# Performance work log

Hardware: AMD Instinct MI355X
Metric: run time of the kernel (lower is better)

The kernel has to match this reference:

```python
import jax, jax.numpy as jnp
import numpy as np

N = 100000   # node_num / batch_node_num (full-graph batch, identity remap)
E = 600000   # edges in adj[nodes, :]
D_IN = 128
D_OUT = 128
MASK = (1.0, 1.0, 0.0, 0.0)  # self-loop mask per `ind` in original forward


def setup_inputs() -> dict:
    key = jax.random.key(0)
    ks = jax.random.split(key, 6)
    feat = jax.random.normal(ks[0], (N, D_IN), dtype=jnp.float32)
    edge_src = jax.random.randint(ks[1], (E,), 0, N)
    edge_dst = jax.random.randint(ks[2], (E,), 0, N)
    W_edge = jax.random.uniform(ks[3], (E,), dtype=jnp.float32)  # W[u][v] per edge
    W1 = jax.random.normal(ks[4], (D_IN, D_OUT), dtype=jnp.float32) / np.sqrt(D_IN).astype(np.float32)
    b1 = jnp.zeros((D_OUT,), jnp.float32)
    W2 = jax.random.normal(ks[5], (D_OUT, D_OUT), dtype=jnp.float32) / np.sqrt(D_OUT).astype(np.float32)
    b2 = jnp.zeros((D_OUT,), jnp.float32)
    return {"feat": feat, "W_edge": W_edge, "W1": W1, "b1": b1, "W2": W2,
            "b2": b2, "edge_src": edge_src, "edge_dst": edge_dst, "ind": 2}


def reference(feat, W_edge, W1, b1, W2, b2, edge_src, edge_dst, ind):
    # values: self-loop edges get mask[ind], others 1 (torch.where on edges[:,0]==edges[:,1])
    mask_val = MASK[ind]  # ind is a static Python int
    values = jnp.where(edge_src == edge_dst, jnp.float32(mask_val), jnp.float32(1.0))
    # degree[v] = row-sum of matrix_coo (spmm with ones); temp_e = degree[dst_e]
    degree = jax.ops.segment_sum(values, edge_src, num_segments=N)
    # new_embeddings = Linear -> Tanh -> Linear on features of (all) unique nodes
    h = jnp.tanh(feat @ W1 + b1) @ W2 + b2  # [N, D_OUT]
    # matrix = matrix_neighbor .* matrix_weight -> per-edge weight degree[dst]*W[u][v]
    w = degree[edge_dst] * W_edge  # [E]
    # results = spmm(matrix, new_embeddings); row_sum = spmm(matrix, ones)
    results = jax.ops.segment_sum(w[:, None] * h[edge_dst], edge_src, num_segments=N)
    row_sum = jax.ops.segment_sum(w, edge_src, num_segments=N)
    row_sum = jnp.where(row_sum == 0, jnp.float32(1.0), row_sum)
    return results / row_sum[:, None]
```

## Files before the change

### kernel.cpp

```cpp
#include <hip/hip_runtime.h>


constexpr int D = 128;
constexpr int MAXDEG = 24;
constexpr int OVF_CAP = 131072;

typedef __attribute__((ext_vector_type(8))) short short8;
typedef __attribute__((ext_vector_type(4))) float f32x4;
struct ushort8_s { unsigned short v[8]; };

__device__ __forceinline__ unsigned short f2bf(float x) {
    unsigned int u = __float_as_uint(x);
    u += 0x7fffu + ((u >> 16) & 1u);
    return (unsigned short)(u >> 16);
}
__device__ __forceinline__ float bflo(unsigned int u) { return __uint_as_float(u << 16); }
__device__ __forceinline__ float bfhi(unsigned int u) { return __uint_as_float(u & 0xffff0000u); }
__device__ __forceinline__ float fast_tanh(float x) {
    float e = exp2f(x * 2.885390081777927f);
    return fmaf(-2.0f, __builtin_amdgcn_rcpf(e + 1.0f), 1.0f);
}
__device__ __forceinline__ int swz(int row, int kbyte) {
    return (row * 256 + kbyte) ^ ((row & 7) << 4);
}

__global__ __launch_bounds__(256) void k_init(const float* __restrict__ W1,
                                              const float* __restrict__ W2,
                                              unsigned short* __restrict__ Wt1s,
                                              unsigned short* __restrict__ Wt2s,
                                              int* __restrict__ zbase, int zv4) {
    int b = blockIdx.x;
    if (b < 64) {
        int t = b * 256 + threadIdx.x;
        int k = t >> 7, nn = t & 127;
        int si = swz(nn, k * 2) >> 1;
        Wt1s[si] = f2bf(W1[t]);
        Wt2s[si] = f2bf(W2[t]);
    } else {
        int i = (b - 64) * 256 + threadIdx.x;
        if (i < zv4) ((int4*)zbase)[i] = make_int4(0, 0, 0, 0);
    }
}

__global__ __launch_bounds__(512, 4) void k_mlp_place(
        const float* __restrict__ feat,
        const unsigned short* __restrict__ Wt1s,
        const unsigned short* __restrict__ Wt2s,
        const float* __restrict__ b1, const float* __restrict__ b2,
        unsigned short* __restrict__ hbf, int n, int nm, int npl,
        const int* __restrict__ src, const int* __restrict__ dst,
        const float* __restrict__ W_edge,
        unsigned int* __restrict__ packed,
        int* __restrict__ ovf_cnt, int4* __restrict__ ovf,
        float2* __restrict__ pairs, int E) {
    __shared__ unsigned short sW1[128 * D];
    __shared__ unsigned short sW2[128 * D];

    const int bid = blockIdx.x;
    bool isMlp;
    int idx;
    if (nm <= npl) {
        if (bid < 2 * nm) { isMlp = !(bid & 1); idx = bid >> 1; }
        else { isMlp = false; idx = nm + (bid - 2 * nm); }
    } else {
        if (bid < 2 * npl) { isMlp = (bid & 1); idx = bid >> 1; }
        else { isMlp = true; idx = npl + (bid - 2 * npl); }
    }

    if (!isMlp) {
        int e = idx * 512 + threadIdx.x;
        if (e < E) {
            int s = src[e];
            int d = dst[e];
            float W = W_edge[e];
            unsigned int add = (s == d) ? 0x10001u : 1u;
            unsigned int old = atomicAdd(&packed[s], add);
            int rank = (int)(old & 0xffffu);
            if (rank < MAXDEG) {
                float2 p;
                p.x = __int_as_float(d);
                p.y = W;
                pairs[(size_t)s * MAXDEG + rank] = p;
            } else {
                int oi = atomicAdd(ovf_cnt, 1);
                if (oi < OVF_CAP) ovf[oi] = make_int4(s, d, __float_as_int(W), 0);
            }
        }
        return;
    }
    const int t = threadIdx.x;
    const int lane = t & 63;
    const int w = t >> 6;
    const int rl0 = w * 16;
    const int row0 = idx * 128 + rl0;
    const int rA = lane & 15;
    const int ks = (lane >> 4) * 8;

    float4 f[4][2];
    {
        int gr = row0 + rA;
        bool ok = gr < n;
        const float* fp = &feat[(size_t)(ok ? gr : 0) * D + ks];
#pragma unroll
        for (int kc = 0; kc < 4; ++kc) {
            f[kc][0] = ok ? *(const float4*)(fp + kc * 32) : make_float4(0.f, 0.f, 0.f, 0.f);
            f[kc][1] = ok ? *(const float4*)(fp + kc * 32 + 4) : make_float4(0.f, 0.f, 0.f, 0.f);
        }
    }

    {
        const ushort8_s* g1 = (const ushort8_s*)Wt1s;
        const ushort8_s* g2 = (const ushort8_s*)Wt2s;
        ushort8_s* l1 = (ushort8_s*)sW1;
        ushort8_s* l2 = (ushort8_s*)sW2;
#pragma unroll
        for (int j = 0; j < 4; ++j) {
            int c = t + j * 512;
            l1[c] = g1[c];
            l2[c] = g2[c];
        }
    }

    float bias1[8], bias2[8];
#pragma unroll
    for (int nf = 0; nf < 8; ++nf) {
        bias1[nf] = b1[nf * 16 + rA];
        bias2[nf] = b2[nf * 16 + rA];
    }

    short8 afrag[4];
#pragma unroll
    for (int kc = 0; kc < 4; ++kc) {
        float4 f0 = f[kc][0], f1 = f[kc][1];
        short8 a;
        a[0] = (short)f2bf(f0.x); a[1] = (short)f2bf(f0.y);
        a[2] = (short)f2bf(f0.z); a[3] = (short)f2bf(f0.w);
        a[4] = (short)f2bf(f1.x); a[5] = (short)f2bf(f1.y);
        a[6] = (short)f2bf(f1.z); a[7] = (short)f2bf(f1.w);
        afrag[kc] = a;
    }

    __syncthreads();

    f32x4 acc[8];
#pragma unroll
    for (int nf = 0; nf < 8; ++nf) acc[nf] = (f32x4){0.f, 0.f, 0.f, 0.f};

#pragma unroll
    for (int kc = 0; kc < 4; ++kc) {
        const int kb = (kc * 32 + ks) * 2;
#pragma unroll
        for (int nf = 0; nf < 8; ++nf) {
            const int rb = nf * 16 + rA;
            short8 b = *(short8*)((char*)sW1 + swz(rb, kb));
            acc[nf] = __builtin_amdgcn_mfma_f32_16x16x32_bf16(afrag[kc], b, acc[nf], 0, 0, 0);
        }
    }

    __syncthreads();

#pragma unroll
    for (int nf = 0; nf < 8; ++nf) {
        const int col = nf * 16 + rA;
#pragma unroll
        for (int i = 0; i < 4; ++i) {
            const int rl = rl0 + (lane >> 4) * 4 + i;
            unsigned short hv = f2bf(fast_tanh(acc[nf][i] + bias1[nf]));
            *(unsigned short*)((char*)sW1 + swz(rl, col * 2)) = hv;
        }
    }

#pragma unroll
    for (int nf = 0; nf < 8; ++nf) acc[nf] = (f32x4){0.f, 0.f, 0.f, 0.f};

#pragma unroll
    for (int kc = 0; kc < 4; ++kc) {
        const int kb = (kc * 32 + ks) * 2;
        const int ra0 = rl0 + rA;
        short8 a0 = *(short8*)((char*)sW1 + swz(ra0, kb));
#pragma unroll
        for (int nf = 0; nf < 8; ++nf) {
            const int rb = nf * 16 + rA;
            short8 b = *(short8*)((char*)sW2 + swz(rb, kb));
            acc[nf] = __builtin_amdgcn_mfma_f32_16x16x32_bf16(a0, b, acc[nf], 0, 0, 0);
        }
    }

#pragma unroll
    for (int nf = 0; nf < 8; ++nf) {
        const int col = nf * 16 + rA;
#pragma unroll
        for (int i = 0; i < 4; ++i) {
            const int rl = rl0 + (lane >> 4) * 4 + i;
            unsigned short hv = f2bf(acc[nf][i] + bias2[nf]);
            *(unsigned short*)((char*)sW1 + swz(rl, col * 2)) = hv;
        }
    }

    for (int c = lane; c < 256; c += 64) {
        int r = c >> 4, k0 = (c & 15) * 8;
        int gr = row0 + r;
        if (gr < n) {
            int rl = rl0 + r;
            short8 v = *(short8*)((char*)sW1 + swz(rl, k0 * 2));
            *(short8*)&hbf[(size_t)gr * D + k0] = v;
        }
    }
}

__global__ __launch_bounds__(256) void k_aggregate(const unsigned int* __restrict__ packed,
                                                   const float2* __restrict__ pairs,
                                                   const int* __restrict__ ovf_cnt,
                                                   const int4* __restrict__ ovf,
                                                   const unsigned short* __restrict__ hbf,
                                                   const int* __restrict__ indp,
                                                   float* __restrict__ out, int n) {
    long long tid = (long long)blockIdx.x * 256 + threadIdx.x;
    int node = (int)(tid >> 4);
    int li = (int)(tid & 15);
    int lane = threadIdx.x & 63;
    if (node >= n) return;
    const float maskm1 = ((indp[0] < 2) ? 1.0f : 0.0f) - 1.0f;

    int cnt = (int)(packed[node] & 0xffffu);
    int mt = (cnt < MAXDEG) ? cnt : MAXDEG;

    float acc[8];
#pragma unroll
    for (int j = 0; j < 8; ++j) acc[j] = 0.f;
    float rsp = 0.f;
    const int gbase = lane & 48;
    const float2* prow = &pairs[(size_t)node * MAXDEG];

    auto fma8 = [&](float w, uint4 h) {
        acc[0] = fmaf(w, bflo(h.x), acc[0]); acc[1] = fmaf(w, bfhi(h.x), acc[1]);
        acc[2] = fmaf(w, bflo(h.y), acc[2]); acc[3] = fmaf(w, bfhi(h.y), acc[3]);
        acc[4] = fmaf(w, bflo(h.z), acc[4]); acc[5] = fmaf(w, bfhi(h.z), acc[5]);
        acc[6] = fmaf(w, bflo(h.w), acc[6]); acc[7] = fmaf(w, bfhi(h.w), acc[7]);
    };

    for (int base = 0; base < mt; base += 16) {
        int mm = mt - base;
        mm = (mm > 16) ? 16 : mm;
        float wv = 0.f;
        float dv = 0.f;
        if (li < mm) {
            float2 p = prow[base + li];
            dv = p.x;
            int d = __float_as_int(p.x);
            unsigned int pkd = packed[d];
            float deg = (float)(pkd & 0xffffu) + maskm1 * (float)(pkd >> 16);
            wv = deg * p.y;
        }
        rsp += wv;
        int i = 0;
        for (; i + 3 < mm; i += 4) {
            int d0 = __float_as_int(__shfl(dv, gbase + i));
            float w0 = __shfl(wv, gbase + i);
            int d1 = __float_as_int(__shfl(dv, gbase + i + 1));
            float w1 = __shfl(wv, gbase + i + 1);
            int d2 = __float_as_int(__shfl(dv, gbase + i + 2));
            float w2 = __shfl(wv, gbase + i + 2);
            int d3 = __float_as_int(__shfl(dv, gbase + i + 3));
            float w3 = __shfl(wv, gbase + i + 3);
            uint4 h0 = *(const uint4*)&hbf[(size_t)d0 * D + li * 8];
            uint4 h1 = *(const uint4*)&hbf[(size_t)d1 * D + li * 8];
            uint4 h2 = *(const uint4*)&hbf[(size_t)d2 * D + li * 8];
            uint4 h3 = *(const uint4*)&hbf[(size_t)d3 * D + li * 8];
            fma8(w0, h0); fma8(w1, h1); fma8(w2, h2); fma8(w3, h3);
        }
        for (; i + 1 < mm; i += 2) {
            int d0 = __float_as_int(__shfl(dv, gbase + i));
            float w0 = __shfl(wv, gbase + i);
            int d1 = __float_as_int(__shfl(dv, gbase + i + 1));
            float w1 = __shfl(wv, gbase + i + 1);
            uint4 h0 = *(const uint4*)&hbf[(size_t)d0 * D + li * 8];
            uint4 h1 = *(const uint4*)&hbf[(size_t)d1 * D + li * 8];
            fma8(w0, h0); fma8(w1, h1);
        }
        if (i < mm) {
            int d0 = __float_as_int(__shfl(dv, gbase + i));
            float w0 = __shfl(wv, gbase + i);
            uint4 h0 = *(const uint4*)&hbf[(size_t)d0 * D + li * 8];
            fma8(w0, h0);
        }
    }

    int ovn = *ovf_cnt;
    if (ovn > OVF_CAP) ovn = OVF_CAP;
    for (int i = 0; i < ovn; ++i) {
        int4 tq = ovf[i];
        if (tq.x == node) {
            int d = tq.y;
            unsigned int pkd = packed[d];
            float deg = (float)(pkd & 0xffffu) + maskm1 * (float)(pkd >> 16);
            float w = deg * __int_as_float(tq.z);
            if (li == 0) rsp += w;
            uint4 h = *(const uint4*)&hbf[(size_t)d * D + li * 8];
            fma8(w, h);
        }
    }

    rsp += __shfl_xor(rsp, 1);
    rsp += __shfl_xor(rsp, 2);
    rsp += __shfl_xor(rsp, 4);
    rsp += __shfl_xor(rsp, 8);
    rsp = (rsp == 0.f) ? 1.f : rsp;
    float inv = 1.0f / rsp;
    float4 o0, o1;
    o0.x = acc[0] * inv; o0.y = acc[1] * inv; o0.z = acc[2] * inv; o0.w = acc[3] * inv;
    o1.x = acc[4] * inv; o1.y = acc[5] * inv; o1.z = acc[6] * inv; o1.w = acc[7] * inv;
    float* op = &out[(size_t)node * D + li * 8];
    *(float4*)op = o0;
    *(float4*)(op + 4) = o1;
}

extern "C" void kernel_launch(void* const* d_in, const int* in_sizes, int n_in,
                              void* d_out, int out_size, void* d_ws, size_t ws_size,
                              hipStream_t stream) {
    const float* feat   = (const float*)d_in[0];
    const float* W_edge = (const float*)d_in[1];
    const float* W1     = (const float*)d_in[2];
    const float* b1     = (const float*)d_in[3];
    const float* W2     = (const float*)d_in[4];
    const float* b2     = (const float*)d_in[5];
    const int* edge_src = (const int*)d_in[6];
    const int* edge_dst = (const int*)d_in[7];
    const int* indp     = (const int*)d_in[8];

    const int n = in_sizes[0] / D;
    const int E = in_sizes[6];

    char* ws = (char*)d_ws;
    unsigned short* Wt1s = (unsigned short*)ws;
    unsigned short* Wt2s = Wt1s + D * D;
    unsigned int* packed = (unsigned int*)(Wt2s + D * D);
    int* ovf_cnt         = (int*)(packed + n);
    int4* ovf            = (int4*)((char*)ovf_cnt + 16);
    float2* pairs        = (float2*)(ovf + OVF_CAP);
    unsigned short* hbf  = (unsigned short*)(pairs + (size_t)n * MAXDEG);

    const int zbytes = n * 4 + 16;
    const int zv4 = zbytes / 16;
    const int zb = (zv4 + 255) / 256;
    k_init<<<64 + zb, 256, 0, stream>>>(W1, W2, Wt1s, Wt2s, (int*)packed, zv4);

    const int nm = (n + 127) / 128;
    const int npl = (E + 511) / 512;
    k_mlp_place<<<nm + npl, 512, 0, stream>>>(feat, Wt1s, Wt2s, b1, b2, hbf, n, nm, npl,
                                              edge_src, edge_dst, W_edge,
                                              packed, ovf_cnt, ovf, pairs, E);

    long long athreads = (long long)n * 16;
    k_aggregate<<<(int)((athreads + 255) / 256), 256, 0, stream>>>(packed, pairs, ovf_cnt,
                                                                   ovf, hbf, indp,
                                                                   (float*)d_out, n);
}
```

Before: 91.04 us.

## Persistent grid-stride aggregation with next-node prefetch; batch edge placement per thread

The aggregate kernel becomes a persistent grid-stride kernel of 2048 blocks. Each 16-lane group handles several nodes and prefetches the next node's count, edge pairs and degree-weighted weights while it accumulates the current node. This hides the dependent packed/pairs latency chain before the gather loop and removes per-node launch overhead, but it also lowers occupancy and adds register pressure. Edge placement blocks now process four edges per thread, cutting the number of scatter blocks fourfold.

```diff
diff --git a/kernel.cpp b/kernel.cpp
--- a/kernel.cpp
+++ b/kernel.cpp
@@ -68,22 +68,26 @@
     }
 
     if (!isMlp) {
-        int e = idx * 512 + threadIdx.x;
-        if (e < E) {
-            int s = src[e];
-            int d = dst[e];
-            float W = W_edge[e];
-            unsigned int add = (s == d) ? 0x10001u : 1u;
-            unsigned int old = atomicAdd(&packed[s], add);
-            int rank = (int)(old & 0xffffu);
-            if (rank < MAXDEG) {
-                float2 p;
-                p.x = __int_as_float(d);
-                p.y = W;
-                pairs[(size_t)s * MAXDEG + rank] = p;
-            } else {
-                int oi = atomicAdd(ovf_cnt, 1);
-                if (oi < OVF_CAP) ovf[oi] = make_int4(s, d, __float_as_int(W), 0);
+        int e0 = idx * 2048 + threadIdx.x;
+#pragma unroll
+        for (int q = 0; q < 4; ++q) {
+            int e = e0 + q * 512;
+            if (e < E) {
+                int s = src[e];
+                int d = dst[e];
+                float W = W_edge[e];
+                unsigned int add = (s == d) ? 0x10001u : 1u;
+                unsigned int old = atomicAdd(&packed[s], add);
+                int rank = (int)(old & 0xffffu);
+                if (rank < MAXDEG) {
+                    float2 p;
+                    p.x = __int_as_float(d);
+                    p.y = W;
+                    pairs[(size_t)s * MAXDEG + rank] = p;
+                } else {
+                    int oi = atomicAdd(ovf_cnt, 1);
+                    if (oi < OVF_CAP) ovf[oi] = make_int4(s, d, __float_as_int(W), 0);
+                }
             }
         }
         return;
@@ -214,55 +218,73 @@
                                                    const int4* __restrict__ ovf,
                                                    const unsigned short* __restrict__ hbf,
                                                    const int* __restrict__ indp,
-                                                   float* __restrict__ out, int n) {
-    long long tid = (long long)blockIdx.x * 256 + threadIdx.x;
-    int node = (int)(tid >> 4);
-    int li = (int)(tid & 15);
-    int lane = threadIdx.x & 63;
-    if (node >= n) return;
+                                                   float* __restrict__ out, int n, int ngroups) {
+    const int li = threadIdx.x & 15;
+    const int lane = threadIdx.x & 63;
+    const int gbase = lane & 48;
+    const int group = (int)(((long long)blockIdx.x * 256 + threadIdx.x) >> 4);
     const float maskm1 = ((indp[0] < 2) ? 1.0f : 0.0f) - 1.0f;
-
-    int cnt = (int)(packed[node] & 0xffffu);
-    int mt = (cnt < MAXDEG) ? cnt : MAXDEG;
+    int ovn = *ovf_cnt;
+    if (ovn > OVF_CAP) ovn = OVF_CAP;
 
     float acc[8];
-#pragma unroll
-    for (int j = 0; j < 8; ++j) acc[j] = 0.f;
-    float rsp = 0.f;
-    const int gbase = lane & 48;
-    const float2* prow = &pairs[(size_t)node * MAXDEG];
-
-    auto fma8 = [&](float w, uint4 h) {
+    auto fma8 = [&acc](float w, uint4 h) {
         acc[0] = fmaf(w, bflo(h.x), acc[0]); acc[1] = fmaf(w, bfhi(h.x), acc[1]);
         acc[2] = fmaf(w, bflo(h.y), acc[2]); acc[3] = fmaf(w, bfhi(h.y), acc[3]);
         acc[4] = fmaf(w, bflo(h.z), acc[4]); acc[5] = fmaf(w, bfhi(h.z), acc[5]);
         acc[6] = fmaf(w, bflo(h.w), acc[6]); acc[7] = fmaf(w, bfhi(h.w), acc[7]);
     };
 
-    for (int base = 0; base < mt; base += 16) {
-        int mm = mt - base;
-        mm = (mm > 16) ? 16 : mm;
-        float wv = 0.f;
-        float dv = 0.f;
-        if (li < mm) {
-            float2 p = prow[base + li];
-            dv = p.x;
-            int d = __float_as_int(p.x);
+    int mtA = 0;
+    float2 pvA = make_float2(0.f, 0.f);
+    float wvA = 0.f;
+    if (group < n) {
+        unsigned int c = packed[group];
+        mtA = (int)(c & 0xffffu);
+        mtA = (mtA < MAXDEG) ? mtA : MAXDEG;
+        pvA = pairs[(size_t)group * MAXDEG + li];
+        int lim = (mtA < 16) ? mtA : 16;
+        if (li < lim) {
+            int d = __float_as_int(pvA.x);
             unsigned int pkd = packed[d];
             float deg = (float)(pkd & 0xffffu) + maskm1 * (float)(pkd >> 16);
-            wv = deg * p.y;
-        }
-        rsp += wv;
+            wvA = deg * pvA.y;
+        }
+    }
+
+    for (int node = group; node < n; node += ngroups) {
+        int nxt = node + ngroups;
+        int mtB = 0;
+        float2 pvB = make_float2(0.f, 0.f);
+        float wvB = 0.f;
+        if (nxt < n) {
+            unsigned int c = packed[nxt];
+            mtB = (int)(c & 0xffffu);
+            mtB = (mtB < MAXDEG) ? mtB : MAXDEG;
+            pvB = pairs[(size_t)nxt * MAXDEG + li];
+            int lim = (mtB < 16) ? mtB : 16;
+            if (li < lim) {
+                int d = __float_as_int(pvB.x);
+                unsigned int pkd = packed[d];
+                float deg = (float)(pkd & 0xffffu) + maskm1 * (float)(pkd >> 16);
+                wvB = deg * pvB.y;
+            }
+        }
+
+#pragma unroll
+        for (int j = 0; j < 8; ++j) acc[j] = 0.f;
+        float rsp = wvA;
+        int mm = (mtA < 16) ? mtA : 16;
         int i = 0;
         for (; i + 3 < mm; i += 4) {
-            int d0 = __float_as_int(__shfl(dv, gbase + i));
-            float w0 = __shfl(wv, gbase + i);
-            int d1 = __float_as_int(__shfl(dv, gbase + i + 1));
-            float w1 = __shfl(wv, gbase + i + 1);
-            int d2 = __float_as_int(__shfl(dv, gbase + i + 2));
-            float w2 = __shfl(wv, gbase + i + 2);
-            int d3 = __float_as_int(__shfl(dv, gbase + i + 3));
-            float w3 = __shfl(wv, gbase + i + 3);
+            int d0 = __float_as_int(__shfl(pvA.x, gbase + i));
+            float w0 = __shfl(wvA, gbase + i);
+            int d1 = __float_as_int(__shfl(pvA.x, gbase + i + 1));
+            float w1 = __shfl(wvA, gbase + i + 1);
+            int d2 = __float_as_int(__shfl(pvA.x, gbase + i + 2));
+            float w2 = __shfl(wvA, gbase + i + 2);
+            int d3 = __float_as_int(__shfl(pvA.x, gbase + i + 3));
+            float w3 = __shfl(wvA, gbase + i + 3);
             uint4 h0 = *(const uint4*)&hbf[(size_t)d0 * D + li * 8];
             uint4 h1 = *(const uint4*)&hbf[(size_t)d1 * D + li * 8];
             uint4 h2 = *(const uint4*)&hbf[(size_t)d2 * D + li * 8];
@@ -270,49 +292,72 @@
             fma8(w0, h0); fma8(w1, h1); fma8(w2, h2); fma8(w3, h3);
         }
         for (; i + 1 < mm; i += 2) {
-            int d0 = __float_as_int(__shfl(dv, gbase + i));
-            float w0 = __shfl(wv, gbase + i);
-            int d1 = __float_as_int(__shfl(dv, gbase + i + 1));
-            float w1 = __shfl(wv, gbase + i + 1);
+            int d0 = __float_as_int(__shfl(pvA.x, gbase + i));
+            float w0 = __shfl(wvA, gbase + i);
+            int d1 = __float_as_int(__shfl(pvA.x, gbase + i + 1));
+            float w1 = __shfl(wvA, gbase + i + 1);
             uint4 h0 = *(const uint4*)&hbf[(size_t)d0 * D + li * 8];
             uint4 h1 = *(const uint4*)&hbf[(size_t)d1 * D + li * 8];
             fma8(w0, h0); fma8(w1, h1);
         }
         if (i < mm) {
-            int d0 = __float_as_int(__shfl(dv, gbase + i));
-            float w0 = __shfl(wv, gbase + i);
+            int d0 = __float_as_int(__shfl(pvA.x, gbase + i));
+            float w0 = __shfl(wvA, gbase + i);
             uint4 h0 = *(const uint4*)&hbf[(size_t)d0 * D + li * 8];
             fma8(w0, h0);
         }
-    }
-
-    int ovn = *ovf_cnt;
-    if (ovn > OVF_CAP) ovn = OVF_CAP;
-    for (int i = 0; i < ovn; ++i) {
-        int4 tq = ovf[i];
-        if (tq.x == node) {
-            int d = tq.y;
-            unsigned int pkd = packed[d];
-            float deg = (float)(pkd & 0xffffu) + maskm1 * (float)(pkd >> 16);
-            float w = deg * __int_as_float(tq.z);
-            if (li == 0) rsp += w;
-            uint4 h = *(const uint4*)&hbf[(size_t)d * D + li * 8];
-            fma8(w, h);
-        }
-    }
-
-    rsp += __shfl_xor(rsp, 1);
-    rsp += __shfl_xor(rsp, 2);
-    rsp += __shfl_xor(rsp, 4);
-    rsp += __shfl_xor(rsp, 8);
-    rsp = (rsp == 0.f) ? 1.f : rsp;
-    float inv = 1.0f / rsp;
-    float4 o0, o1;
-    o0.x = acc[0] * inv; o0.y = acc[1] * inv; o0.z = acc[2] * inv; o0.w = acc[3] * inv;
-    o1.x = acc[4] * inv; o1.y = acc[5] * inv; o1.z = acc[6] * inv; o1.w = acc[7] * inv;
-    float* op = &out[(size_t)node * D + li * 8];
-    *(float4*)op = o0;
-    *(float4*)(op + 4) = o1;
+
+        if (mtA > 16) {
+            const float2* prow = &pairs[(size_t)node * MAXDEG];
+            int rem = mtA - 16;
+            float wv2 = 0.f, dv2 = 0.f;
+            if (li < rem) {
+                float2 p = prow[16 + li];
+                dv2 = p.x;
+                int d = __float_as_int(p.x);
+                unsigned int pkd = packed[d];
+                float deg = (float)(pkd & 0xffffu) + maskm1 * (float)(pkd >> 16);
+                wv2 = deg * p.y;
+            }
+            rsp += wv2;
+            for (int i2 = 0; i2 < rem; ++i2) {
+                int d0 = __float_as_int(__shfl(dv2, gbase + i2));
+                float w0 = __shfl(wv2, gbase + i2);
+                uint4 h0 = *(const uint4*)&hbf[(size_t)d0 * D + li * 8];
+                fma8(w0, h0);
+            }
+        }
+
+        if (ovn > 0) {
+            for (int k = 0; k < ovn; ++k) {
+                int4 tq = ovf[k];
+                if (tq.x == node) {
+                    int d = tq.y;
+                    unsigned int pkd = packed[d];
+                    float deg = (float)(pkd & 0xffffu) + maskm1 * (float)(pkd >> 16);
+                    float wq = deg * __int_as_float(tq.z);
+                    if (li == 0) rsp += wq;
+                    uint4 h = *(const uint4*)&hbf[(size_t)d * D + li * 8];
+                    fma8(wq, h);
+                }
+            }
+        }
+
+        rsp += __shfl_xor(rsp, 1);
+        rsp += __shfl_xor(rsp, 2);
+        rsp += __shfl_xor(rsp, 4);
+        rsp += __shfl_xor(rsp, 8);
+        rsp = (rsp == 0.f) ? 1.f : rsp;
+        float inv = 1.0f / rsp;
+        float4 o0, o1;
+        o0.x = acc[0] * inv; o0.y = acc[1] * inv; o0.z = acc[2] * inv; o0.w = acc[3] * inv;
+        o1.x = acc[4] * inv; o1.y = acc[5] * inv; o1.z = acc[6] * inv; o1.w = acc[7] * inv;
+        float* op = &out[(size_t)node * D + li * 8];
+        *(float4*)op = o0;
+        *(float4*)(op + 4) = o1;
+
+        mtA = mtB; pvA = pvB; wvA = wvB;
+    }
 }
 
 extern "C" void kernel_launch(void* const* d_in, const int* in_sizes, int n_in,
@@ -346,13 +391,13 @@
     k_init<<<64 + zb, 256, 0, stream>>>(W1, W2, Wt1s, Wt2s, (int*)packed, zv4);
 
     const int nm = (n + 127) / 128;
-    const int npl = (E + 511) / 512;
+    const int npl = (E + 2047) / 2048;
     k_mlp_place<<<nm + npl, 512, 0, stream>>>(feat, Wt1s, Wt2s, b1, b2, hbf, n, nm, npl,
                                               edge_src, edge_dst, W_edge,
                                               packed, ovf_cnt, ovf, pairs, E);
 
-    long long athreads = (long long)n * 16;
-    k_aggregate<<<(int)((athreads + 255) / 256), 256, 0, stream>>>(packed, pairs, ovf_cnt,
-                                                                   ovf, hbf, indp,
-                                                                   (float*)d_out, n);
-}
+    const int ab = 2048;
+    const int ngroups = ab * 16;
+    k_aggregate<<<ab, 256, 0, stream>>>(packed, pairs, ovf_cnt, ovf, hbf, indp,
+                                        (float*)d_out, n, ngroups);
+}
```

Result: slower. 97.44 us (+7.0%).

## Fuse edge placement into MLP blocks to overlap atomics with matmul

Applied to the files above, without the earlier changes.

Edge placement no longer runs in separate blocks. Each MLP block now also handles its own slice of edges, up to 1024 per block. The edge loads and atomics are issued early, the MLP compute then hides their latency, and the pair writes happen at the end with nontemporal stores. This removes the extra block scheduling and lets memory latency overlap with compute, but it adds register pressure and ties edge throughput to the MLP block count. Correctness depends on epb <= 1024, which holds for E=600000 and nm=782.

```diff
diff --git a/kernel.cpp b/kernel.cpp
--- a/kernel.cpp
+++ b/kernel.cpp
@@ -47,54 +47,31 @@
         const unsigned short* __restrict__ Wt1s,
         const unsigned short* __restrict__ Wt2s,
         const float* __restrict__ b1, const float* __restrict__ b2,
-        unsigned short* __restrict__ hbf, int n, int nm, int npl,
+        unsigned short* __restrict__ hbf, int n,
         const int* __restrict__ src, const int* __restrict__ dst,
         const float* __restrict__ W_edge,
         unsigned int* __restrict__ packed,
         int* __restrict__ ovf_cnt, int4* __restrict__ ovf,
-        float2* __restrict__ pairs, int E) {
+        float2* __restrict__ pairs, int E, int epb) {
     __shared__ unsigned short sW1[128 * D];
     __shared__ unsigned short sW2[128 * D];
-
-    const int bid = blockIdx.x;
-    bool isMlp;
-    int idx;
-    if (nm <= npl) {
-        if (bid < 2 * nm) { isMlp = !(bid & 1); idx = bid >> 1; }
-        else { isMlp = false; idx = nm + (bid - 2 * nm); }
-    } else {
-        if (bid < 2 * npl) { isMlp = (bid & 1); idx = bid >> 1; }
-        else { isMlp = true; idx = npl + (bid - 2 * npl); }
-    }
-
-    if (!isMlp) {
-        int e = idx * 512 + threadIdx.x;
-        if (e < E) {
-            int s = src[e];
-            int d = dst[e];
-            float W = W_edge[e];
-            unsigned int add = (s == d) ? 0x10001u : 1u;
-            unsigned int old = atomicAdd(&packed[s], add);
-            int rank = (int)(old & 0xffffu);
-            if (rank < MAXDEG) {
-                float2 p;
-                p.x = __int_as_float(d);
-                p.y = W;
-                pairs[(size_t)s * MAXDEG + rank] = p;
-            } else {
-                int oi = atomicAdd(ovf_cnt, 1);
-                if (oi < OVF_CAP) ovf[oi] = make_int4(s, d, __float_as_int(W), 0);
-            }
-        }
-        return;
-    }
     const int t = threadIdx.x;
     const int lane = t & 63;
     const int w = t >> 6;
     const int rl0 = w * 16;
-    const int row0 = idx * 128 + rl0;
+    const int row0 = blockIdx.x * 128 + rl0;
     const int rA = lane & 15;
     const int ks = (lane >> 4) * 8;
+
+    const int ebase = blockIdx.x * epb;
+    const int e1 = ebase + t;
+    const int e2 = e1 + 512;
+    const bool v1 = (t < epb) && (e1 < E);
+    const bool v2 = (t < epb - 512) && (e2 < E);
+    int s1 = 0, d1 = 0, s2 = 0, d2 = 0;
+    float ew1 = 0.f, ew2 = 0.f;
+    if (v1) { s1 = src[e1]; d1 = dst[e1]; ew1 = W_edge[e1]; }
+    if (v2) { s2 = src[e2]; d2 = dst[e2]; ew2 = W_edge[e2]; }
 
     float4 f[4][2];
     {
@@ -120,6 +97,10 @@
             l2[c] = g2[c];
         }
     }
+
+    unsigned int old1 = 0, old2 = 0;
+    if (v1) old1 = atomicAdd(&packed[s1], (s1 == d1) ? 0x10001u : 1u);
+    if (v2) old2 = atomicAdd(&packed[s2], (s2 == d2) ? 0x10001u : 1u);
 
     float bias1[8], bias2[8];
 #pragma unroll
@@ -204,6 +185,31 @@
             int rl = rl0 + r;
             short8 v = *(short8*)((char*)sW1 + swz(rl, k0 * 2));
             *(short8*)&hbf[(size_t)gr * D + k0] = v;
+        }
+    }
+
+    if (v1) {
+        int rank = (int)(old1 & 0xffffu);
+        if (rank < MAXDEG) {
+            unsigned long long pk =
+                (unsigned long long)(unsigned int)d1 |
+                ((unsigned long long)__float_as_uint(ew1) << 32);
+            __builtin_nontemporal_store(pk, (unsigned long long*)&pairs[(size_t)s1 * MAXDEG + rank]);
+        } else {
+            int oi = atomicAdd(ovf_cnt, 1);
+            if (oi < OVF_CAP) ovf[oi] = make_int4(s1, d1, __float_as_int(ew1), 0);
+        }
+    }
+    if (v2) {
+        int rank = (int)(old2 & 0xffffu);
+        if (rank < MAXDEG) {
+            unsigned long long pk =
+                (unsigned long long)(unsigned int)d2 |
+                ((unsigned long long)__float_as_uint(ew2) << 32);
+            __builtin_nontemporal_store(pk, (unsigned long long*)&pairs[(size_t)s2 * MAXDEG + rank]);
+        } else {
+            int oi = atomicAdd(ovf_cnt, 1);
+            if (oi < OVF_CAP) ovf[oi] = make_int4(s2, d2, __float_as_int(ew2), 0);
         }
     }
 }
@@ -346,10 +352,10 @@
     k_init<<<64 + zb, 256, 0, stream>>>(W1, W2, Wt1s, Wt2s, (int*)packed, zv4);
 
     const int nm = (n + 127) / 128;
-    const int npl = (E + 511) / 512;
-    k_mlp_place<<<nm + npl, 512, 0, stream>>>(feat, Wt1s, Wt2s, b1, b2, hbf, n, nm, npl,
-                                              edge_src, edge_dst, W_edge,
-                                              packed, ovf_cnt, ovf, pairs, E);
+    const int epb = (E + nm - 1) / nm;
+    k_mlp_place<<<nm, 512, 0, stream>>>(feat, Wt1s, Wt2s, b1, b2, hbf, n,
+                                        edge_src, edge_dst, W_edge,
+                                        packed, ovf_cnt, ovf, pairs, E, epb);
 
     long long athreads = (long long)n * 16;
     k_aggregate<<<(int)((athreads + 255) / 256), 256, 0, stream>>>(packed, pairs, ovf_cnt,
```

New measurement: 98.47 us. 1.08x slower.
